# Kernel tuning notes

Measured on AMD Instinct MI355X. Metric: run time of the kernel, lower is better.

## Reference

```python
import jax, jax.numpy as jnp
import numpy as np

B = 64          # number of jets
LVLS = 13       # tree levels (complete binary tree, 4096 leaves/jet)
F = 7           # input features
H = 64          # hidden size
SIZES = [B * (2 ** j) for j in range(LVLS)]
OFFS = np.concatenate([[0], np.cumsum(SIZES)])  # level offsets into flat contents


def setup_inputs() -> dict:
    key = jax.random.key(0)
    ks = jax.random.split(key, 9)
    n_total = int(OFFS[-1])  # 524224
    s = lambda k, shp, fan: jax.random.normal(k, shp, jnp.float32) / np.sqrt(fan)
    return {
        "contents": jax.random.normal(ks[0], (n_total, F), jnp.float32),
        "W_u": s(ks[1], (H, F), F),       "b_u": jnp.zeros((H,), jnp.float32),
        "W_r": s(ks[2], (3 * H, 3 * H), 3 * H), "b_r": jnp.zeros((3 * H,), jnp.float32),
        "W_h": s(ks[3], (H, 3 * H), 3 * H),     "b_h": jnp.zeros((H,), jnp.float32),
        "W_z": s(ks[4], (4 * H, 4 * H), 4 * H), "b_z": jnp.zeros((4 * H,), jnp.float32),
    }


def reference(contents, W_u, b_u, W_r, b_r, W_h, b_h, W_z, b_z):
    # Bottom-up recursive gated embedding (n_iters=0 path -> relu activation).
    up = None  # embedding of level j+1
    for j in reversed(range(LVLS)):
        c = contents[int(OFFS[j]):int(OFFS[j + 1])]        # [n_j, F]
        u = jax.nn.relu(c @ W_u.T + b_u)                   # [n_j, H]
        if j == LVLS - 1:
            up = u                                         # leaf level: no inners
            continue
        n = SIZES[j]
        # children of node k are (2k, 2k+1) at level j+1 -> strided gather
        h_L = up[0::2]                                     # [n_j, H]
        h_R = up[1::2]                                     # [n_j, H]
        hhu = jnp.concatenate([h_L, h_R, u], axis=1)       # [n_j, 3H]
        r = jax.nn.sigmoid(hhu @ W_r.T + b_r)              # reset gate
        h_H = jax.nn.relu((r * hhu) @ W_h.T + b_h)         # candidate
        z = jnp.concatenate([h_H, hhu], axis=1) @ W_z.T + b_z  # [n_j, 4H]
        g = jax.nn.softmax(z.reshape(n, 4, H), axis=1)     # softmax over 4 gates
        up = g[:, 0] * h_H + g[:, 1] * h_L + g[:, 2] * h_R + g[:, 3] * u
    return up.reshape(B, -1)                               # [B, H]
```

## Files before the change

### kernel.cpp

```cpp
#include <hip/hip_runtime.h>
#include <hip/hip_bf16.h>


#define LOG2E 1.4426950408889634f
#define OSTR 76

typedef __bf16 bf16x8 __attribute__((ext_vector_type(8)));
typedef unsigned short u16x8 __attribute__((ext_vector_type(8)));
typedef float f32x4 __attribute__((ext_vector_type(4)));
typedef unsigned short bfr;

__device__ __forceinline__ float bfr2f(bfr v) { return __uint_as_float(((unsigned)v) << 16); }
__device__ __forceinline__ bfr f2bfr(float f) {
    __hip_bfloat16 h = __float2bfloat16(f);
    return __builtin_bit_cast(bfr, h);
}
__device__ __forceinline__ float fexp2(float x) {
#if __has_builtin(__builtin_amdgcn_exp2f)
    return __builtin_amdgcn_exp2f(x);
#else
    return exp2f(x);
#endif
}
__device__ __forceinline__ float frcp(float x) {
#if __has_builtin(__builtin_amdgcn_rcpf)
    return __builtin_amdgcn_rcpf(x);
#else
    return 1.f / x;
#endif
}

__device__ __forceinline__ int fidx(int Mt, int kt, int q, int ln, int KT) {
    return ((((Mt * KT + kt) * 4 + q) * 16 + ln) * 8);
}

__device__ __host__ __forceinline__ size_t lvloff(int j) {
    return (size_t)((64 << j) - 64) * 64;
}

__device__ __forceinline__ void pack_one(const float* __restrict__ W, bfr* __restrict__ dst,
                                         int d, int K, float scale) {
    int KT = K >> 5;
    int j = d & 7, lnc = (d >> 3) & 15, q = (d >> 7) & 3;
    int t1 = d >> 9;
    int kt = t1 % KT, ntile = t1 / KT;
    int ncol = ntile * 16 + lnc;
    int k = kt * 32 + q * 8 + j;
    dst[d] = f2bfr(W[(size_t)ncol * K + k] * scale);
}

__global__ void convert_weights(const float* __restrict__ Wr, const float* __restrict__ Wh,
                                const float* __restrict__ Wz, const float* __restrict__ Wu,
                                const float* __restrict__ br, const float* __restrict__ bz,
                                bfr* __restrict__ wr, bfr* __restrict__ wh, bfr* __restrict__ wz,
                                bfr* __restrict__ wu,
                                float* __restrict__ brs, float* __restrict__ bzs) {
    int i = blockIdx.x * 256 + threadIdx.x;
    if (i < 36864) pack_one(Wr, wr, i, 192, LOG2E);
    if (i < 12288) pack_one(Wh, wh, i, 192, 1.f);
    if (i < 65536) pack_one(Wz, wz, i, 256, LOG2E);
    if (i < 2048) {
        int j = i & 7, lnc = (i >> 3) & 15, q = (i >> 7) & 3, ntile = i >> 9;
        int k = q * 8 + j, ncol = ntile * 16 + lnc;
        wu[i] = (k < 7) ? f2bfr(Wu[ncol * 7 + k]) : (bfr)0;
    }
    if (i < 192) brs[i] = br[i] * LOG2E;
    if (i < 256) bzs[i] = bz[i] * LOG2E;
}

__global__ void convert_contents(const float* __restrict__ c, bfr* __restrict__ c16) {
    int i = blockIdx.x * 256 + threadIdx.x;
    if (i < 524224) {
        const float* cp = c + (size_t)i * 7;
        ushort v[8];
#pragma unroll
        for (int k = 0; k < 7; ++k) v[k] = f2bfr(cp[k]);
        v[7] = 0;
        *(uint4*)&c16[(size_t)i * 8] = *(const uint4*)v;
    }
}

__device__ __forceinline__ void stage_c16(const bfr* __restrict__ c16src, int rows,
                                          bfr* s_c) {
    const int tid = threadIdx.x;
    for (int t = tid; t < rows * 4; t += 256) {
        int row = t >> 2, qg = t & 3;
        uint4 v = {0u, 0u, 0u, 0u};
        if (qg == 0) v = *(const uint4*)&c16src[(size_t)row * 8];
        *(uint4*)&s_c[(((row >> 4) * 4 + qg) * 16 + (row & 15)) * 8] = v;
    }
}

__device__ __forceinline__ bf16x8 load_c_frag16(const bfr* __restrict__ c16,
                                                size_t grow, bool active) {
    uint4 v = {0u, 0u, 0u, 0u};
    if (active) v = *(const uint4*)&c16[grow * 8];
    return __builtin_bit_cast(bf16x8, v);
}

__device__ __forceinline__ void store_up_coalesced(
    int row0, int rows, bfr* __restrict__ u_io,
    const ushort (&ovv)[4][4], int Mtn, bfr* s_t)
{
    const int tid = threadIdx.x;
    const int lane = tid & 63, w = tid >> 6;
    const int ln = lane & 15, q = lane >> 4;
    const int colbase = w * 16 + q * 4;
    __syncthreads();
#pragma unroll
    for (int Mt = 0; Mt < 4; ++Mt) {
        if (Mt < Mtn) {
            int row = Mt * 16 + ln;
            if (row < rows)
                *(uint2*)&s_t[row * OSTR + colbase] = *(const uint2*)ovv[Mt];
        }
    }
    __syncthreads();
#pragma unroll
    for (int it = 0; it < 2; ++it) {
        int idx = it * 256 + tid;
        int row = idx >> 3, ck = idx & 7;
        if (row < rows)
            *(uint4*)&u_io[(size_t)(row0 + row) * 64 + ck * 8] =
                *(const uint4*)&s_t[row * OSTR + ck * 8];
    }
}

__device__ __forceinline__ void mmu_own(const bfr* s_c, bfr* s_hhu, bf16x8 awu,
                                        f32x4 bu4, int Mtn, int ln, int q,
                                        int colbase) {
#pragma unroll
    for (int Mt = 0; Mt < 4; ++Mt) {
        if (Mt < Mtn) {
            bf16x8 Bc = *(const bf16x8*)&s_c[((Mt * 4 + q) * 16 + ln) * 8];
            f32x4 acc = {0.f, 0.f, 0.f, 0.f};
            acc = __builtin_amdgcn_mfma_f32_16x16x32_bf16(awu, Bc, acc, 0, 0, 0);
            int kk = 128 + colbase;
            int addr = fidx(Mt, kk >> 5, (kk >> 3) & 3, ln, 6) + (kk & 7);
            ushort uv[4];
#pragma unroll
            for (int r = 0; r < 4; ++r) uv[r] = f2bfr(fmaxf(acc[r] + bu4[r], 0.f));
            *(uint2*)&s_hhu[addr] = *(const uint2*)uv;
        }
    }
}

template <bool CHILD_U>
__device__ __forceinline__ void tile_glob(
    int row0,
    const bfr* __restrict__ ch, const bfr* __restrict__ c16_child,
    const bfr* __restrict__ c16_own, bfr* __restrict__ u_io,
    const bfr* __restrict__ wu, const float* __restrict__ b_u,
    const bfr* __restrict__ wr, const float* __restrict__ brs,
    const bfr* __restrict__ wh, const float* __restrict__ b_h,
    const bfr* __restrict__ wz, const float* __restrict__ bzs,
    bfr* s_hhu, bfr* s_t)
{
    bfr* s_hH = s_t;
    const int tid = threadIdx.x;
    const int lane = tid & 63, w = tid >> 6;
    const int ln = lane & 15, q = lane >> 4;
    const int colbase = w * 16 + q * 4;

    if (!CHILD_U) {
#pragma unroll
        for (int it = 0; it < 4; ++it) {
            int idx = it * 256 + tid;
            int lns = idx & 15, qs = (idx >> 4) & 3, kts = (idx >> 6) & 3, Mts = idx >> 8;
            int row = Mts * 16 + lns;
            int k = kts * 32 + qs * 8;
            const bfr* src = (k < 64)
                ? ch + (size_t)(2 * (row0 + row)) * 64 + k
                : ch + (size_t)(2 * (row0 + row) + 1) * 64 + (k - 64);
            *(uint4*)&s_hhu[fidx(Mts, kts, qs, lns, 6)] = *(const uint4*)src;
        }
    } else {
        stage_c16(c16_child + (size_t)(2 * row0) * 8, 128, s_t + 2048);
    }
    stage_c16(c16_own + (size_t)row0 * 8, 64, s_t);
    __syncthreads();

    {
        bf16x8 awu = *(const bf16x8*)&wu[fidx(w, 0, q, ln, 1)];
        f32x4 bu4 = *(const f32x4*)&b_u[colbase];
        if (CHILD_U) {
#pragma unroll
            for (int Mt = 0; Mt < 8; ++Mt) {
                bf16x8 Bc = *(const bf16x8*)&s_t[2048 + (((Mt * 4 + q) * 16 + ln) * 8)];
                f32x4 acc = {0.f, 0.f, 0.f, 0.f};
                acc = __builtin_amdgcn_mfma_f32_16x16x32_bf16(awu, Bc, acc, 0, 0, 0);
                int crow = Mt * 16 + ln;
                int row = crow >> 1;
                int kk = (crow & 1) * 64 + colbase;
                int addr = fidx(row >> 4, kk >> 5, (kk >> 3) & 3, row & 15, 6) + (kk & 7);
                ushort uv[4];
#pragma unroll
                for (int r = 0; r < 4; ++r) uv[r] = f2bfr(fmaxf(acc[r] + bu4[r], 0.f));
                *(uint2*)&s_hhu[addr] = *(const uint2*)uv;
            }
        }
        mmu_own(s_t, s_hhu, awu, bu4, 4, ln, q, colbase);
    }
    __syncthreads();

    {
        bf16x8 Af[3][6];
#pragma unroll
        for (int nt = 0; nt < 3; ++nt)
#pragma unroll
            for (int kt = 0; kt < 6; ++kt)
                Af[nt][kt] = *(const bf16x8*)&wr[fidx(w * 3 + nt, kt, q, ln, 6)];
#pragma unroll
        for (int Mt = 0; Mt < 4; ++Mt) {
            bf16x8 Bf[6];
#pragma unroll
            for (int kt = 0; kt < 6; ++kt)
                Bf[kt] = *(const bf16x8*)&s_hhu[fidx(Mt, kt, q, ln, 6)];
#pragma unroll
            for (int nt = 0; nt < 3; ++nt) {
                int cb1 = (w * 3 + nt) * 16 + q * 4;
                f32x4 acc = {0.f, 0.f, 0.f, 0.f};
#pragma unroll
                for (int kt = 0; kt < 6; ++kt)
                    acc = __builtin_amdgcn_mfma_f32_16x16x32_bf16(Af[nt][kt], Bf[kt], acc, 0, 0, 0);
                f32x4 br4 = *(const f32x4*)&brs[cb1];
                int addr = fidx(Mt, cb1 >> 5, (cb1 >> 3) & 3, ln, 6) + (cb1 & 7);
                ushort hh[4], tt[4];
                *(uint2*)hh = *(const uint2*)&s_hhu[addr];
#pragma unroll
                for (int r = 0; r < 4; ++r) {
                    float e = fexp2(-(acc[r] + br4[r]));
                    tt[r] = f2bfr(frcp(1.f + e) * bfr2f(hh[r]));
                }
                *(uint2*)&s_t[addr] = *(const uint2*)tt;
            }
        }
    }
    __syncthreads();

    f32x4 hacc[4];
    {
        bf16x8 Ah[6];
#pragma unroll
        for (int kt = 0; kt < 6; ++kt)
            Ah[kt] = *(const bf16x8*)&wh[fidx(w, kt, q, ln, 6)];
#pragma unroll
        for (int Mt = 0; Mt < 4; ++Mt) {
            f32x4 acc = {0.f, 0.f, 0.f, 0.f};
#pragma unroll
            for (int kt = 0; kt < 6; ++kt) {
                bf16x8 Bf = *(const bf16x8*)&s_t[fidx(Mt, kt, q, ln, 6)];
                acc = __builtin_amdgcn_mfma_f32_16x16x32_bf16(Ah[kt], Bf, acc, 0, 0, 0);
            }
            hacc[Mt] = acc;
        }
    }
    __syncthreads();
    {
        f32x4 bh4 = *(const f32x4*)&b_h[colbase];
#pragma unroll
        for (int Mt = 0; Mt < 4; ++Mt) {
            int addr = fidx(Mt, colbase >> 5, (colbase >> 3) & 3, ln, 2) + (colbase & 7);
            ushort hv[4];
#pragma unroll
            for (int r = 0; r < 4; ++r) hv[r] = f2bfr(fmaxf(hacc[Mt][r] + bh4[r], 0.f));
            *(uint2*)&s_hH[addr] = *(const uint2*)hv;
        }
    }
    __syncthreads();

    {
        f32x4 az[4][4];
#pragma unroll
        for (int Mt = 0; Mt < 4; ++Mt)
#pragma unroll
            for (int g = 0; g < 4; ++g) az[Mt][g] = (f32x4){0.f, 0.f, 0.f, 0.f};
#pragma unroll
        for (int g = 0; g < 4; ++g) {
            bf16x8 Aw[8];
#pragma unroll
            for (int kt = 0; kt < 8; ++kt)
                Aw[kt] = *(const bf16x8*)&wz[fidx(g * 4 + w, kt, q, ln, 8)];
#pragma unroll
            for (int Mt = 0; Mt < 4; ++Mt) {
                f32x4 acc = az[Mt][g];
                acc = __builtin_amdgcn_mfma_f32_16x16x32_bf16(
                    Aw[0], *(const bf16x8*)&s_hH[fidx(Mt, 0, q, ln, 2)], acc, 0, 0, 0);
                acc = __builtin_amdgcn_mfma_f32_16x16x32_bf16(
                    Aw[1], *(const bf16x8*)&s_hH[fidx(Mt, 1, q, ln, 2)], acc, 0, 0, 0);
#pragma unroll
                for (int kt = 0; kt < 6; ++kt)
                    acc = __builtin_amdgcn_mfma_f32_16x16x32_bf16(
                        Aw[2 + kt], *(const bf16x8*)&s_hhu[fidx(Mt, kt, q, ln, 6)], acc, 0, 0, 0);
                az[Mt][g] = acc;
            }
        }
        f32x4 bz0 = *(const f32x4*)&bzs[colbase];
        f32x4 bz1 = *(const f32x4*)&bzs[64 + colbase];
        f32x4 bz2 = *(const f32x4*)&bzs[128 + colbase];
        f32x4 bz3 = *(const f32x4*)&bzs[192 + colbase];
        ushort ovv[4][4];
#pragma unroll
        for (int Mt = 0; Mt < 4; ++Mt) {
            int aH = fidx(Mt, colbase >> 5, (colbase >> 3) & 3, ln, 2) + (colbase & 7);
            int a0 = fidx(Mt, colbase >> 5, (colbase >> 3) & 3, ln, 6) + (colbase & 7);
            int c1 = 64 + colbase, c2 = 128 + colbase;
            int a1 = fidx(Mt, c1 >> 5, (c1 >> 3) & 3, ln, 6) + (c1 & 7);
            int a2 = fidx(Mt, c2 >> 5, (c2 >> 3) & 3, ln, 6) + (c2 & 7);
            ushort hHv[4], u0[4], u1[4], u2[4];
            *(uint2*)hHv = *(const uint2*)&s_hH[aH];
            *(uint2*)u0 = *(const uint2*)&s_hhu[a0];
            *(uint2*)u1 = *(const uint2*)&s_hhu[a1];
            *(uint2*)u2 = *(const uint2*)&s_hhu[a2];
#pragma unroll
            for (int r = 0; r < 4; ++r) {
                float e0 = fexp2(az[Mt][0][r] + bz0[r]);
                float e1 = fexp2(az[Mt][1][r] + bz1[r]);
                float e2 = fexp2(az[Mt][2][r] + bz2[r]);
                float e3 = fexp2(az[Mt][3][r] + bz3[r]);
                float inv = frcp(e0 + e1 + e2 + e3);
                float v = (e0 * bfr2f(hHv[r]) + e1 * bfr2f(u0[r]) +
                           e2 * bfr2f(u1[r]) + e3 * bfr2f(u2[r])) * inv;
                ovv[Mt][r] = f2bfr(v);
            }
        }
        store_up_coalesced(row0, 64, u_io, ovv, 4, s_t);
    }
}

__global__ __launch_bounds__(256, 2) void level11_kernel(
    const bfr* __restrict__ c16_12, const bfr* __restrict__ c16_11,
    bfr* __restrict__ u_io,
    const bfr* __restrict__ wr, const float* __restrict__ brs,
    const bfr* __restrict__ wh, const float* __restrict__ b_h,
    const bfr* __restrict__ wz, const float* __restrict__ bzs,
    const bfr* __restrict__ wu, const float* __restrict__ b_u)
{
    __shared__ bfr s_hhu[12288];
    __shared__ bfr s_t[12288];
    tile_glob<true>(blockIdx.x * 64, nullptr, c16_12, c16_11, u_io,
                    wu, b_u, wr, brs, wh, b_h, wz, bzs, s_hhu, s_t);
}

__global__ __launch_bounds__(256, 2) void level_kernel(
    const bfr* __restrict__ ch, const bfr* __restrict__ c16_own,
    bfr* __restrict__ u_io,
    const bfr* __restrict__ wr, const float* __restrict__ brs,
    const bfr* __restrict__ wh, const float* __restrict__ b_h,
    const bfr* __restrict__ wz, const float* __restrict__ bzs,
    const bfr* __restrict__ wu, const float* __restrict__ b_u)
{
    __shared__ bfr s_hhu[12288];
    __shared__ bfr s_t[12288];
    tile_glob<false>(blockIdx.x * 64, ch, nullptr, c16_own, u_io,
                     wu, b_u, wr, brs, wh, b_h, wz, bzs, s_hhu, s_t);
}

__device__ __forceinline__ void load_wregs(
    const bfr* __restrict__ wr, const bfr* __restrict__ wh, const bfr* __restrict__ wz,
    const bfr* __restrict__ wu, int w, int q, int ln,
    bf16x8 (&Af)[3][6], bf16x8 (&Ah)[6], bf16x8 (&Aw)[4][8], bf16x8& awu)
{
#pragma unroll
    for (int nt = 0; nt < 3; ++nt)
#pragma unroll
        for (int kt = 0; kt < 6; ++kt)
            Af[nt][kt] = *(const bf16x8*)&wr[fidx(w * 3 + nt, kt, q, ln, 6)];
#pragma unroll
    for (int kt = 0; kt < 6; ++kt)
        Ah[kt] = *(const bf16x8*)&wh[fidx(w, kt, q, ln, 6)];
#pragma unroll
    for (int g = 0; g < 4; ++g)
#pragma unroll
        for (int kt = 0; kt < 8; ++kt)
            Aw[g][kt] = *(const bf16x8*)&wz[fidx(g * 4 + w, kt, q, ln, 8)];
    awu = *(const bf16x8*)&wu[fidx(w, 0, q, ln, 1)];
}

__device__ __forceinline__ void tile_regs(
    int row0, int rows,
    const bfr* __restrict__ ch, const bfr* __restrict__ c16_own,
    bfr* __restrict__ u_io,
    const bf16x8 awu, const float* __restrict__ b_u,
    const bf16x8 (&Af)[3][6], const bf16x8 (&Ah)[6], const bf16x8 (&Aw)[4][8],
    const float* __restrict__ brs, const float* __restrict__ b_h,
    const float* __restrict__ bzs,
    float* __restrict__ outp, bfr* s_hhu, bfr* s_t, bfr* s_hH)
{
    const int tid = threadIdx.x;
    const int lane = tid & 63, w = tid >> 6;
    const int ln = lane & 15, q = lane >> 4;
    const int Mtn = (rows + 15) >> 4;
    const int colbase = w * 16 + q * 4;

    __syncthreads();

#pragma unroll
    for (int it = 0; it < 4; ++it) {
        int idx = it * 256 + tid;
        int lns = idx & 15, qs = (idx >> 4) & 3, kts = (idx >> 6) & 3, Mts = idx >> 8;
        int row = Mts * 16 + lns;
        if (row < rows) {
            int k = kts * 32 + qs * 8;
            const bfr* src = (k < 64)
                ? ch + (size_t)(2 * (row0 + row)) * 64 + k
                : ch + (size_t)(2 * (row0 + row) + 1) * 64 + (k - 64);
            *(uint4*)&s_hhu[fidx(Mts, kts, qs, lns, 6)] = *(const uint4*)src;
        }
    }
    {
        f32x4 bu4 = *(const f32x4*)&b_u[colbase];
#pragma unroll
        for (int Mt = 0; Mt < 4; ++Mt) {
            if (Mt < Mtn) {
                int row = Mt * 16 + ln;
                bf16x8 Bc = load_c_frag16(c16_own, (size_t)row0 + row, q == 0 && row < rows);
                f32x4 acc = {0.f, 0.f, 0.f, 0.f};
                acc = __builtin_amdgcn_mfma_f32_16x16x32_bf16(awu, Bc, acc, 0, 0, 0);
                int kk = 128 + colbase;
                int addr = fidx(Mt, kk >> 5, (kk >> 3) & 3, ln, 6) + (kk & 7);
                ushort uv[4];
#pragma unroll
                for (int r = 0; r < 4; ++r) uv[r] = f2bfr(fmaxf(acc[r] + bu4[r], 0.f));
                *(uint2*)&s_hhu[addr] = *(const uint2*)uv;
            }
        }
    }
    __syncthreads();

#pragma unroll
    for (int Mt = 0; Mt < 4; ++Mt) {
        if (Mt < Mtn) {
            bf16x8 Bf[6];
#pragma unroll
            for (int kt = 0; kt < 6; ++kt)
                Bf[kt] = *(const bf16x8*)&s_hhu[fidx(Mt, kt, q, ln, 6)];
#pragma unroll
            for (int nt = 0; nt < 3; ++nt) {
                int cb1 = (w * 3 + nt) * 16 + q * 4;
                f32x4 acc = {0.f, 0.f, 0.f, 0.f};
#pragma unroll
                for (int kt = 0; kt < 6; ++kt)
                    acc = __builtin_amdgcn_mfma_f32_16x16x32_bf16(Af[nt][kt], Bf[kt], acc, 0, 0, 0);
                f32x4 br4 = *(const f32x4*)&brs[cb1];
                int addr = fidx(Mt, cb1 >> 5, (cb1 >> 3) & 3, ln, 6) + (cb1 & 7);
                ushort hh[4], tt[4];
                *(uint2*)hh = *(const uint2*)&s_hhu[addr];
#pragma unroll
                for (int r = 0; r < 4; ++r) {
                    float e = fexp2(-(acc[r] + br4[r]));
                    tt[r] = f2bfr(frcp(1.f + e) * bfr2f(hh[r]));
                }
                *(uint2*)&s_t[addr] = *(const uint2*)tt;
            }
        }
    }
    __syncthreads();

    {
        f32x4 bh4 = *(const f32x4*)&b_h[colbase];
#pragma unroll
        for (int Mt = 0; Mt < 4; ++Mt) {
            if (Mt < Mtn) {
                f32x4 acc = {0.f, 0.f, 0.f, 0.f};
#pragma unroll
                for (int kt = 0; kt < 6; ++kt) {
                    bf16x8 Bf = *(const bf16x8*)&s_t[fidx(Mt, kt, q, ln, 6)];
                    acc = __builtin_amdgcn_mfma_f32_16x16x32_bf16(Ah[kt], Bf, acc, 0, 0, 0);
                }
                int addr = fidx(Mt, colbase >> 5, (colbase >> 3) & 3, ln, 2) + (colbase & 7);
                ushort hv[4];
#pragma unroll
                for (int r = 0; r < 4; ++r) hv[r] = f2bfr(fmaxf(acc[r] + bh4[r], 0.f));
                *(uint2*)&s_hH[addr] = *(const uint2*)hv;
            }
        }
    }
    __syncthreads();

    {
        f32x4 bz0 = *(const f32x4*)&bzs[colbase];
        f32x4 bz1 = *(const f32x4*)&bzs[64 + colbase];
        f32x4 bz2 = *(const f32x4*)&bzs[128 + colbase];
        f32x4 bz3 = *(const f32x4*)&bzs[192 + colbase];
#pragma unroll
        for (int Mt = 0; Mt < 4; ++Mt) {
            if (Mt < Mtn) {
                bf16x8 Az[8];
                Az[0] = *(const bf16x8*)&s_hH[fidx(Mt, 0, q, ln, 2)];
                Az[1] = *(const bf16x8*)&s_hH[fidx(Mt, 1, q, ln, 2)];
#pragma unroll
                for (int kt = 0; kt < 6; ++kt)
                    Az[2 + kt] = *(const bf16x8*)&s_hhu[fidx(Mt, kt, q, ln, 6)];
                f32x4 azg[4];
#pragma unroll
                for (int g = 0; g < 4; ++g) {
                    f32x4 acc = {0.f, 0.f, 0.f, 0.f};
#pragma unroll
                    for (int kt = 0; kt < 8; ++kt)
                        acc = __builtin_amdgcn_mfma_f32_16x16x32_bf16(Aw[g][kt], Az[kt], acc, 0, 0, 0);
                    azg[g] = acc;
                }
                int row = Mt * 16 + ln;
                if (row < rows) {
                    int aH = fidx(Mt, colbase >> 5, (colbase >> 3) & 3, ln, 2) + (colbase & 7);
                    int a0 = fidx(Mt, colbase >> 5, (colbase >> 3) & 3, ln, 6) + (colbase & 7);
                    int c1 = 64 + colbase, c2 = 128 + colbase;
                    int a1 = fidx(Mt, c1 >> 5, (c1 >> 3) & 3, ln, 6) + (c1 & 7);
                    int a2 = fidx(Mt, c2 >> 5, (c2 >> 3) & 3, ln, 6) + (c2 & 7);
                    ushort hHv[4], u0[4], u1[4], u2[4], ov[4];
                    *(uint2*)hHv = *(const uint2*)&s_hH[aH];
                    *(uint2*)u0 = *(const uint2*)&s_hhu[a0];
                    *(uint2*)u1 = *(const uint2*)&s_hhu[a1];
                    *(uint2*)u2 = *(const uint2*)&s_hhu[a2];
                    float of[4];
#pragma unroll
                    for (int r = 0; r < 4; ++r) {
                        float e0 = fexp2(azg[0][r] + bz0[r]);
                        float e1 = fexp2(azg[1][r] + bz1[r]);
                        float e2 = fexp2(azg[2][r] + bz2[r]);
                        float e3 = fexp2(azg[3][r] + bz3[r]);
                        float inv = frcp(e0 + e1 + e2 + e3);
                        float v = (e0 * bfr2f(hHv[r]) + e1 * bfr2f(u0[r]) +
                                   e2 * bfr2f(u1[r]) + e3 * bfr2f(u2[r])) * inv;
                        ov[r] = f2bfr(v); of[r] = v;
                    }
                    *(uint2*)&s_t[row * OSTR + colbase] = *(const uint2*)ov;
                    if (outp)
                        *(float4*)&outp[(size_t)(row0 + row) * 64 + colbase] = *(const float4*)of;
                }
            }
        }
    }
    __syncthreads();
    {
        const int tid2 = threadIdx.x;
#pragma unroll
        for (int it = 0; it < 2; ++it) {
            int idx = it * 256 + tid2;
            int row = idx >> 3, ck = idx & 7;
            if (row < rows)
                *(uint4*)&u_io[(size_t)(row0 + row) * 64 + ck * 8] =
                    *(const uint4*)&s_t[row * OSTR + ck * 8];
        }
    }
}

__global__ __launch_bounds__(256, 1) void fused_mid_regs(
    const bfr* __restrict__ c16, bfr* __restrict__ u_all,
    const bfr* __restrict__ wr, const float* __restrict__ brs,
    const bfr* __restrict__ wh, const float* __restrict__ b_h,
    const bfr* __restrict__ wz, const float* __restrict__ bzs,
    const bfr* __restrict__ wu, const float* __restrict__ b_u)
{
    __shared__ bfr s_hhu[12288];
    __shared__ bfr s_t[12288];
    __shared__ bfr s_hH[4096];
    const int tid = threadIdx.x;
    const int lane = tid & 63, w = tid >> 6, ln = lane & 15, q = lane >> 4;
    bf16x8 Af[3][6], Ah[6], Aw[4][8], awu;
    load_wregs(wr, wh, wz, wu, w, q, ln, Af, Ah, Aw, awu);
    for (int j = 8; j >= 2; --j) {
        int rows = 1 << (j - 2);
        const bfr* c16_own = c16 + (size_t)((64 << j) - 64) * 8;
        tile_regs(blockIdx.x * rows, rows,
                  u_all + lvloff(j + 1), c16_own, u_all + lvloff(j),
                  awu, b_u, Af, Ah, Aw, brs, b_h, bzs,
                  nullptr, s_hhu, s_t, s_hH);
    }
}

__global__ __launch_bounds__(256, 1) void fused_tail_regs(
    const bfr* __restrict__ c16, bfr* __restrict__ u_all,
    const bfr* __restrict__ wr, const float* __restrict__ brs,
    const bfr* __restrict__ wh, const float* __restrict__ b_h,
    const bfr* __restrict__ wz, const float* __restrict__ bzs,
    const bfr* __restrict__ wu, const float* __restrict__ b_u,
    float* __restrict__ outp)
{
    __shared__ bfr s_hhu[12288];
    __shared__ bfr s_t[12288];
    __shared__ bfr s_hH[4096];
    const int tid = threadIdx.x;
    const int lane = tid & 63, w = tid >> 6, ln = lane & 15, q = lane >> 4;
    bf16x8 Af[3][6], Ah[6], Aw[4][8], awu;
    load_wregs(wr, wh, wz, wu, w, q, ln, Af, Ah, Aw, awu);
    for (int j = 1; j >= 0; --j) {
        int rows = 1 << j;
        const bfr* c16_own = c16 + (size_t)((64 << j) - 64) * 8;
        tile_regs(blockIdx.x * rows, rows,
                  u_all + lvloff(j + 1), c16_own, u_all + lvloff(j),
                  awu, b_u, Af, Ah, Aw, brs, b_h, bzs,
                  (j == 0) ? outp : nullptr, s_hhu, s_t, s_hH);
    }
}

extern "C" void kernel_launch(void* const* d_in, const int* in_sizes, int n_in,
                              void* d_out, int out_size, void* d_ws, size_t ws_size,
                              hipStream_t stream) {
    const float* contents = (const float*)d_in[0];
    const float* W_u = (const float*)d_in[1];
    const float* b_u = (const float*)d_in[2];
    const float* W_r = (const float*)d_in[3];
    const float* b_r = (const float*)d_in[4];
    const float* W_h = (const float*)d_in[5];
    const float* b_h = (const float*)d_in[6];
    const float* W_z = (const float*)d_in[7];
    const float* b_z = (const float*)d_in[8];
    float* out = (float*)d_out;

    bfr* u_all = (bfr*)d_ws;
    bfr* wr = u_all + (size_t)524224 * 64;
    bfr* wh = wr + 36864;
    bfr* wz = wh + 12288;
    float* brs = (float*)(wz + 65536);
    float* bzs = brs + 192;
    bfr* wu = (bfr*)(bzs + 256);
    bfr* c16 = u_all + lvloff(12);

    convert_weights<<<256, 256, 0, stream>>>(W_r, W_h, W_z, W_u, b_r, b_z,
                                             wr, wh, wz, wu, brs, bzs);
    convert_contents<<<2048, 256, 0, stream>>>(contents, c16);

    const bfr* c16_12 = c16 + (size_t)((64 << 12) - 64) * 8;
    const bfr* c16_11 = c16 + (size_t)((64 << 11) - 64) * 8;
    const bfr* c16_10 = c16 + (size_t)((64 << 10) - 64) * 8;
    const bfr* c16_9  = c16 + (size_t)((64 << 9)  - 64) * 8;

    level11_kernel<<<2048, 256, 0, stream>>>(c16_12, c16_11, u_all + lvloff(11),
                                             wr, brs, wh, b_h, wz, bzs, wu, b_u);
    level_kernel<<<1024, 256, 0, stream>>>(u_all + lvloff(11), c16_10, u_all + lvloff(10),
                                           wr, brs, wh, b_h, wz, bzs, wu, b_u);
    level_kernel<<<512, 256, 0, stream>>>(u_all + lvloff(10), c16_9, u_all + lvloff(9),
                                          wr, brs, wh, b_h, wz, bzs, wu, b_u);
    fused_mid_regs<<<256, 256, 0, stream>>>(c16, u_all,
                                            wr, brs, wh, b_h, wz, bzs, wu, b_u);
    fused_tail_regs<<<64, 256, 0, stream>>>(c16, u_all,
                                            wr, brs, wh, b_h, wz, bzs, wu, b_u, out);
}
```

Baseline: 198.9 us.

## Merge conversion kernels and drop LDS staging for contents and outputs

Fuses the weight and contents conversion kernels into a single launch, removing one kernel launch. In tile_glob, contents fragments are loaded straight from global memory into MFMA operands instead of being staged through shared memory first, which removes a barrier. Output rows are written directly from registers as 8-byte stores instead of being transposed through LDS for coalesced 16-byte stores. This trades store coalescing for fewer barriers and less LDS traffic.

```diff
diff --git a/kernel.cpp b/kernel.cpp
--- a/kernel.cpp
+++ b/kernel.cpp
@@ -3,7 +3,6 @@
 
 
 #define LOG2E 1.4426950408889634f
-#define OSTR 76
 
 typedef __bf16 bf16x8 __attribute__((ext_vector_type(8)));
 typedef unsigned short u16x8 __attribute__((ext_vector_type(8)));
@@ -49,13 +48,23 @@
     dst[d] = f2bfr(W[(size_t)ncol * K + k] * scale);
 }
 
-__global__ void convert_weights(const float* __restrict__ Wr, const float* __restrict__ Wh,
-                                const float* __restrict__ Wz, const float* __restrict__ Wu,
-                                const float* __restrict__ br, const float* __restrict__ bz,
-                                bfr* __restrict__ wr, bfr* __restrict__ wh, bfr* __restrict__ wz,
-                                bfr* __restrict__ wu,
-                                float* __restrict__ brs, float* __restrict__ bzs) {
+__global__ void convert_inputs(
+    const float* __restrict__ c, bfr* __restrict__ c16,
+    const float* __restrict__ Wr, const float* __restrict__ Wh,
+    const float* __restrict__ Wz, const float* __restrict__ Wu,
+    const float* __restrict__ br, const float* __restrict__ bz,
+    bfr* __restrict__ wr, bfr* __restrict__ wh, bfr* __restrict__ wz,
+    bfr* __restrict__ wu, float* __restrict__ brs, float* __restrict__ bzs)
+{
     int i = blockIdx.x * 256 + threadIdx.x;
+    if (i < 524224) {
+        const float* cp = c + (size_t)i * 7;
+        ushort v[8];
+#pragma unroll
+        for (int k = 0; k < 7; ++k) v[k] = f2bfr(cp[k]);
+        v[7] = 0;
+        *(uint4*)&c16[(size_t)i * 8] = *(const uint4*)v;
+    }
     if (i < 36864) pack_one(Wr, wr, i, 192, LOG2E);
     if (i < 12288) pack_one(Wh, wh, i, 192, 1.f);
     if (i < 65536) pack_one(Wz, wz, i, 256, LOG2E);
@@ -68,81 +77,11 @@
     if (i < 256) bzs[i] = bz[i] * LOG2E;
 }
 
-__global__ void convert_contents(const float* __restrict__ c, bfr* __restrict__ c16) {
-    int i = blockIdx.x * 256 + threadIdx.x;
-    if (i < 524224) {
-        const float* cp = c + (size_t)i * 7;
-        ushort v[8];
-#pragma unroll
-        for (int k = 0; k < 7; ++k) v[k] = f2bfr(cp[k]);
-        v[7] = 0;
-        *(uint4*)&c16[(size_t)i * 8] = *(const uint4*)v;
-    }
-}
-
-__device__ __forceinline__ void stage_c16(const bfr* __restrict__ c16src, int rows,
-                                          bfr* s_c) {
-    const int tid = threadIdx.x;
-    for (int t = tid; t < rows * 4; t += 256) {
-        int row = t >> 2, qg = t & 3;
-        uint4 v = {0u, 0u, 0u, 0u};
-        if (qg == 0) v = *(const uint4*)&c16src[(size_t)row * 8];
-        *(uint4*)&s_c[(((row >> 4) * 4 + qg) * 16 + (row & 15)) * 8] = v;
-    }
-}
-
-__device__ __forceinline__ bf16x8 load_c_frag16(const bfr* __restrict__ c16,
-                                                size_t grow, bool active) {
+__device__ __forceinline__ bf16x8 c16_frag(const bfr* __restrict__ c16,
+                                           size_t grow, bool active) {
     uint4 v = {0u, 0u, 0u, 0u};
     if (active) v = *(const uint4*)&c16[grow * 8];
     return __builtin_bit_cast(bf16x8, v);
-}
-
-__device__ __forceinline__ void store_up_coalesced(
-    int row0, int rows, bfr* __restrict__ u_io,
-    const ushort (&ovv)[4][4], int Mtn, bfr* s_t)
-{
-    const int tid = threadIdx.x;
-    const int lane = tid & 63, w = tid >> 6;
-    const int ln = lane & 15, q = lane >> 4;
-    const int colbase = w * 16 + q * 4;
-    __syncthreads();
-#pragma unroll
-    for (int Mt = 0; Mt < 4; ++Mt) {
-        if (Mt < Mtn) {
-            int row = Mt * 16 + ln;
-            if (row < rows)
-                *(uint2*)&s_t[row * OSTR + colbase] = *(const uint2*)ovv[Mt];
-        }
-    }
-    __syncthreads();
-#pragma unroll
-    for (int it = 0; it < 2; ++it) {
-        int idx = it * 256 + tid;
-        int row = idx >> 3, ck = idx & 7;
-        if (row < rows)
-            *(uint4*)&u_io[(size_t)(row0 + row) * 64 + ck * 8] =
-                *(const uint4*)&s_t[row * OSTR + ck * 8];
-    }
-}
-
-__device__ __forceinline__ void mmu_own(const bfr* s_c, bfr* s_hhu, bf16x8 awu,
-                                        f32x4 bu4, int Mtn, int ln, int q,
-                                        int colbase) {
-#pragma unroll
-    for (int Mt = 0; Mt < 4; ++Mt) {
-        if (Mt < Mtn) {
-            bf16x8 Bc = *(const bf16x8*)&s_c[((Mt * 4 + q) * 16 + ln) * 8];
-            f32x4 acc = {0.f, 0.f, 0.f, 0.f};
-            acc = __builtin_amdgcn_mfma_f32_16x16x32_bf16(awu, Bc, acc, 0, 0, 0);
-            int kk = 128 + colbase;
-            int addr = fidx(Mt, kk >> 5, (kk >> 3) & 3, ln, 6) + (kk & 7);
-            ushort uv[4];
-#pragma unroll
-            for (int r = 0; r < 4; ++r) uv[r] = f2bfr(fmaxf(acc[r] + bu4[r], 0.f));
-            *(uint2*)&s_hhu[addr] = *(const uint2*)uv;
-        }
-    }
 }
 
 template <bool CHILD_U>
@@ -174,22 +113,17 @@
                 : ch + (size_t)(2 * (row0 + row) + 1) * 64 + (k - 64);
             *(uint4*)&s_hhu[fidx(Mts, kts, qs, lns, 6)] = *(const uint4*)src;
         }
-    } else {
-        stage_c16(c16_child + (size_t)(2 * row0) * 8, 128, s_t + 2048);
-    }
-    stage_c16(c16_own + (size_t)row0 * 8, 64, s_t);
-    __syncthreads();
-
+    }
     {
         bf16x8 awu = *(const bf16x8*)&wu[fidx(w, 0, q, ln, 1)];
         f32x4 bu4 = *(const f32x4*)&b_u[colbase];
         if (CHILD_U) {
 #pragma unroll
             for (int Mt = 0; Mt < 8; ++Mt) {
-                bf16x8 Bc = *(const bf16x8*)&s_t[2048 + (((Mt * 4 + q) * 16 + ln) * 8)];
+                int crow = Mt * 16 + ln;
+                bf16x8 Bc = c16_frag(c16_child, (size_t)(2 * row0) + crow, q == 0);
                 f32x4 acc = {0.f, 0.f, 0.f, 0.f};
                 acc = __builtin_amdgcn_mfma_f32_16x16x32_bf16(awu, Bc, acc, 0, 0, 0);
-                int crow = Mt * 16 + ln;
                 int row = crow >> 1;
                 int kk = (crow & 1) * 64 + colbase;
                 int addr = fidx(row >> 4, kk >> 5, (kk >> 3) & 3, row & 15, 6) + (kk & 7);
@@ -199,7 +133,18 @@
                 *(uint2*)&s_hhu[addr] = *(const uint2*)uv;
             }
         }
-        mmu_own(s_t, s_hhu, awu, bu4, 4, ln, q, colbase);
+#pragma unroll
+        for (int Mt = 0; Mt < 4; ++Mt) {
+            bf16x8 Bc = c16_frag(c16_own, (size_t)row0 + Mt * 16 + ln, q == 0);
+            f32x4 acc = {0.f, 0.f, 0.f, 0.f};
+            acc = __builtin_amdgcn_mfma_f32_16x16x32_bf16(awu, Bc, acc, 0, 0, 0);
+            int kk = 128 + colbase;
+            int addr = fidx(Mt, kk >> 5, (kk >> 3) & 3, ln, 6) + (kk & 7);
+            ushort uv[4];
+#pragma unroll
+            for (int r = 0; r < 4; ++r) uv[r] = f2bfr(fmaxf(acc[r] + bu4[r], 0.f));
+            *(uint2*)&s_hhu[addr] = *(const uint2*)uv;
+        }
     }
     __syncthreads();
 
@@ -299,7 +244,6 @@
         f32x4 bz1 = *(const f32x4*)&bzs[64 + colbase];
         f32x4 bz2 = *(const f32x4*)&bzs[128 + colbase];
         f32x4 bz3 = *(const f32x4*)&bzs[192 + colbase];
-        ushort ovv[4][4];
 #pragma unroll
         for (int Mt = 0; Mt < 4; ++Mt) {
             int aH = fidx(Mt, colbase >> 5, (colbase >> 3) & 3, ln, 2) + (colbase & 7);
@@ -307,7 +251,7 @@
             int c1 = 64 + colbase, c2 = 128 + colbase;
             int a1 = fidx(Mt, c1 >> 5, (c1 >> 3) & 3, ln, 6) + (c1 & 7);
             int a2 = fidx(Mt, c2 >> 5, (c2 >> 3) & 3, ln, 6) + (c2 & 7);
-            ushort hHv[4], u0[4], u1[4], u2[4];
+            ushort hHv[4], u0[4], u1[4], u2[4], ov[4];
             *(uint2*)hHv = *(const uint2*)&s_hH[aH];
             *(uint2*)u0 = *(const uint2*)&s_hhu[a0];
             *(uint2*)u1 = *(const uint2*)&s_hhu[a1];
@@ -321,10 +265,11 @@
                 float inv = frcp(e0 + e1 + e2 + e3);
                 float v = (e0 * bfr2f(hHv[r]) + e1 * bfr2f(u0[r]) +
                            e2 * bfr2f(u1[r]) + e3 * bfr2f(u2[r])) * inv;
-                ovv[Mt][r] = f2bfr(v);
-            }
-        }
-        store_up_coalesced(row0, 64, u_io, ovv, 4, s_t);
+                ov[r] = f2bfr(v);
+            }
+            *(uint2*)&u_io[(size_t)(row0 + Mt * 16 + ln) * 64 + colbase] =
+                *(const uint2*)ov;
+        }
     }
 }
 
@@ -414,7 +359,7 @@
         for (int Mt = 0; Mt < 4; ++Mt) {
             if (Mt < Mtn) {
                 int row = Mt * 16 + ln;
-                bf16x8 Bc = load_c_frag16(c16_own, (size_t)row0 + row, q == 0 && row < rows);
+                bf16x8 Bc = c16_frag(c16_own, (size_t)row0 + row, q == 0 && row < rows);
                 f32x4 acc = {0.f, 0.f, 0.f, 0.f};
                 acc = __builtin_amdgcn_mfma_f32_16x16x32_bf16(awu, Bc, acc, 0, 0, 0);
                 int kk = 128 + colbase;
@@ -525,23 +470,12 @@
                                    e2 * bfr2f(u1[r]) + e3 * bfr2f(u2[r])) * inv;
                         ov[r] = f2bfr(v); of[r] = v;
                     }
-                    *(uint2*)&s_t[row * OSTR + colbase] = *(const uint2*)ov;
+                    *(uint2*)&u_io[(size_t)(row0 + row) * 64 + colbase] =
+                        *(const uint2*)ov;
                     if (outp)
                         *(float4*)&outp[(size_t)(row0 + row) * 64 + colbase] = *(const float4*)of;
                 }
             }
-        }
-    }
-    __syncthreads();
-    {
-        const int tid2 = threadIdx.x;
-#pragma unroll
-        for (int it = 0; it < 2; ++it) {
-            int idx = it * 256 + tid2;
-            int row = idx >> 3, ck = idx & 7;
-            if (row < rows)
-                *(uint4*)&u_io[(size_t)(row0 + row) * 64 + ck * 8] =
-                    *(const uint4*)&s_t[row * OSTR + ck * 8];
         }
     }
 }
@@ -618,9 +552,9 @@
     bfr* wu = (bfr*)(bzs + 256);
     bfr* c16 = u_all + lvloff(12);
 
-    convert_weights<<<256, 256, 0, stream>>>(W_r, W_h, W_z, W_u, b_r, b_z,
+    convert_inputs<<<2048, 256, 0, stream>>>(contents, c16,
+                                             W_r, W_h, W_z, W_u, b_r, b_z,
                                              wr, wh, wz, wu, brs, bzs);
-    convert_contents<<<2048, 256, 0, stream>>>(contents, c16);
 
     const bfr* c16_12 = c16 + (size_t)((64 << 12) - 64) * 8;
     const bfr* c16_11 = c16 + (size_t)((64 << 11) - 64) * 8;
```

After: 209.1 us. 5.1% more time.
